# Optimization experiments

Measured on AMD Instinct MI355X. Metric: run time of the kernel, lower is better.

## Reference

```python
import jax, jax.numpy as jnp
import numpy as np

NUM_HEADS = 12
DIM = 768
NV = 4  # number of views
EPS = 1e-6


def _ln(x, g, b):
    m = x.mean(-1, keepdims=True)
    v = ((x - m) ** 2).mean(-1, keepdims=True)
    return (x - m) / jnp.sqrt(v + EPS) * g + b


def setup_inputs() -> dict:
    key = jax.random.key(0)
    ks = jax.random.split(key, 10)
    B, N, C, H = 4, 256, DIM, NUM_HEADS
    Hid = 4 * C
    s = 0.02
    return {
        'X': jax.random.normal(ks[0], (B * NV, N, C), jnp.float32),
        'norm1_g': jnp.ones((C,), jnp.float32),
        'norm1_b': jnp.zeros((C,), jnp.float32),
        'qkv_w': jax.random.normal(ks[1], (NV, 3 * C, C), jnp.float32) * s,
        'proj_w': jax.random.normal(ks[2], (NV, C, C), jnp.float32) * s,
        'proj_b': jnp.zeros((NV, C), jnp.float32),
        'norm2_g': jnp.ones((NV, C), jnp.float32),
        'norm2_b': jnp.zeros((NV, C), jnp.float32),
        'fc1_w': jax.random.normal(ks[3], (NV, Hid, C), jnp.float32) * s,
        'fc1_b': jnp.zeros((NV, Hid), jnp.float32),
        'fc2_w': jax.random.normal(ks[4], (NV, C, Hid), jnp.float32) * s,
        'fc2_b': jnp.zeros((NV, C), jnp.float32),
        'query': jax.random.normal(ks[5], (1, 1, C), jnp.float32),
        'mha_in_w': jax.random.normal(ks[6], (NV, 3 * C, C), jnp.float32) * s,
        'mha_in_b': jnp.zeros((NV, 3 * C), jnp.float32),
        'mha_out_w': jax.random.normal(ks[7], (NV, C, C), jnp.float32) * s,
        'mha_out_b': jnp.zeros((NV, C), jnp.float32),
    }


def reference(X, norm1_g, norm1_b, qkv_w, proj_w, proj_b, norm2_g, norm2_b,
              fc1_w, fc1_b, fc2_w, fc2_b, query, mha_in_w, mha_in_b,
              mha_out_w, mha_out_b):
    B4, N, C = X.shape
    B = B4 // NV
    H = NUM_HEADS
    hd = C // H
    scale = hd ** -0.5

    Xv = X.reshape(B, NV, N, C)
    Xn = _ln(Xv, norm1_g, norm1_b)

    # ---- FusionAttention: 4x4 pairwise cross attention between views ----
    qkv = jnp.einsum('bvnc,vdc->vbnd', Xn, qkv_w)              # [V,B,N,3C]
    qkv = qkv.reshape(NV, B, N, 3, H, hd).transpose(3, 0, 1, 4, 2, 5)  # [3,V,B,H,N,hd]
    q, k, v = qkv[0], qkv[1], qkv[2]
    scores = jnp.einsum('ibhnd,jbhmd->ijbhnm', q, k) * scale   # [V,V,B,H,N,N]
    attn = jax.nn.softmax(scores, axis=-1)
    ctx = jnp.einsum('ijbhnm,jbhmd->ijbhnd', attn, v)
    ctx = ctx.transpose(0, 1, 2, 4, 3, 5).reshape(NV, NV, B, N, C)
    # proj_i is affine, so mean over j of proj(x_j) == proj(mean_j x_j)
    ctx_mean = ctx.mean(axis=1)                                # [V,B,N,C]
    xa = jnp.einsum('vbnc,voc->vbno', ctx_mean, proj_w) + proj_b[:, None, None, :]

    x = xa * 2.0
    h = _ln(x, norm2_g[:, None, None, :], norm2_b[:, None, None, :])
    h1 = jax.nn.gelu(jnp.einsum('vbnc,vhc->vbnh', h, fc1_w) + fc1_b[:, None, None, :],
                     approximate=False)
    h2 = jnp.einsum('vbnh,vch->vbnc', h1, fc2_w) + fc2_b[:, None, None, :]
    x = x + h2                                                  # [V,B,N,C]

    # ---- CrossAttentionWithLearnableQuery (query identical for all T,B) ----
    wq, wk, wv = jnp.split(mha_in_w, 3, axis=1)                 # each [V,C,C]
    bq, bk, bv = jnp.split(mha_in_b, 3, axis=1)                 # each [V,C]
    q0 = query.reshape(C)
    qh = (jnp.einsum('c,vdc->vd', q0, wq) + bq).reshape(NV, H, hd)
    kh = (jnp.einsum('vbnc,vdc->vbnd', x, wk) + bk[:, None, None, :]).reshape(NV, B, N, H, hd)
    vh = (jnp.einsum('vbnc,vdc->vbnd', x, wv) + bv[:, None, None, :]).reshape(NV, B, N, H, hd)
    s2 = jnp.einsum('vhd,vbnhd->vbhn', qh, kh) * scale
    a2 = jax.nn.softmax(s2, axis=-1)
    c2 = jnp.einsum('vbhn,vbnhd->vbhd', a2, vh).reshape(NV, B, C)
    o = jnp.einsum('vbc,voc->vbo', c2, mha_out_w) + mha_out_b[:, None, :]  # [V,B,C]
    o = o.transpose(1, 0, 2).reshape(B, NV * C)                 # concat views
    # every query position produces identical output -> broadcast over T=N
    return jnp.broadcast_to(o[:, None, :], (B, N, NV * C))
```

## Files before the change

kernel.cpp:

```cpp
#include <hip/hip_runtime.h>
#include <math.h>

#define NVIEW 4
#define BATCH 4
#define NSEQ  256
#define CDIM  768
#define HEADS 12
#define HD    64

typedef __attribute__((ext_vector_type(8))) short   short8;
typedef __attribute__((ext_vector_type(8))) unsigned short ushort8;
typedef __attribute__((ext_vector_type(4))) float   float4v;

typedef const __attribute__((address_space(1))) void gas_t;
typedef       __attribute__((address_space(3))) void las_t;

__device__ __forceinline__ unsigned short f2b(float x)
{
    union { float f; unsigned u; } c; c.f = x;
    unsigned r = (c.u + 0x7FFFu + ((c.u >> 16) & 1u)) >> 16;
    return (unsigned short)r;
}

__device__ __forceinline__ unsigned pack2b(float a, float b)
{
    return (unsigned)f2b(a) | ((unsigned)f2b(b) << 16);
}

__device__ __forceinline__ void block_ln_row_b(const float* __restrict__ xrow,
                                               const float* __restrict__ g,
                                               const float* __restrict__ b,
                                               unsigned short* __restrict__ orow)
{
    const int t = threadIdx.x;
    float x0 = xrow[t], x1 = xrow[t + 256], x2 = xrow[t + 512];
    float s  = x0 + x1 + x2;
    float s2 = x0 * x0 + x1 * x1 + x2 * x2;
    #pragma unroll
    for (int off = 32; off > 0; off >>= 1) {
        s  += __shfl_down(s, off);
        s2 += __shfl_down(s2, off);
    }
    __shared__ float w1[4], w2[4];
    if ((t & 63) == 0) { w1[t >> 6] = s; w2[t >> 6] = s2; }
    __syncthreads();
    float S  = w1[0] + w1[1] + w1[2] + w1[3];
    float S2 = w2[0] + w2[1] + w2[2] + w2[3];
    float mean = S * (1.0f / 768.0f);
    float var  = S2 * (1.0f / 768.0f) - mean * mean;
    float inv  = rsqrtf(var + 1e-6f);
    orow[t]       = f2b((x0 - mean) * inv * g[t]       + b[t]);
    orow[t + 256] = f2b((x1 - mean) * inv * g[t + 256] + b[t + 256]);
    orow[t + 512] = f2b((x2 - mean) * inv * g[t + 512] + b[t + 512]);
}

__global__ void prologue(const float* __restrict__ X, const float* __restrict__ n1g,
                         const float* __restrict__ n1b, unsigned short* __restrict__ Xn,
                         const float* __restrict__ query, const float* __restrict__ Win,
                         const float* __restrict__ Bin, float* __restrict__ QH,
                         const float* __restrict__ qkv, const float* __restrict__ proj,
                         const float* __restrict__ fc1, const float* __restrict__ fc2,
                         const float* __restrict__ mha, unsigned short* __restrict__ wdst)
{
    const int bid = blockIdx.x;
    const int t   = threadIdx.x;

    if (bid < 4096) {
        const long NV8 = 4423680L;
        long vi = (long)bid * 256 + t;
        #pragma unroll 2
        for (; vi < NV8; vi += 4096L * 256) {
            long idx = vi * 8;
            const float* s;
            long base;
            if (idx < 7077888L)       { s = qkv;  base = 0; }
            else if (idx < 9437184L)  { s = proj; base = 7077888L; }
            else if (idx < 18874368L) { s = fc1;  base = 9437184L; }
            else if (idx < 28311552L) { s = fc2;  base = 18874368L; }
            else                      { s = mha;  base = 28311552L; }
            const float* sp = s + (idx - base);
            float4 a = *(const float4*)sp;
            float4 b = *(const float4*)(sp + 4);
            ushort8 o;
            o[0] = f2b(a.x); o[1] = f2b(a.y); o[2] = f2b(a.z); o[3] = f2b(a.w);
            o[4] = f2b(b.x); o[5] = f2b(b.y); o[6] = f2b(b.z); o[7] = f2b(b.w);
            *(ushort8*)(wdst + idx) = o;
        }
        return;
    }

    if (bid < 8192) {
        int rid = bid - 4096;
        int n  = rid & 255;
        int bv = rid >> 8;
        int bb = bv >> 2, v = bv & 3;
        const float* xrow = X + (long)rid * CDIM;
        unsigned short* orow = Xn + ((long)(v * 4 + bb) * 256 + n) * CDIM;
        block_ln_row_b(xrow, n1g, n1b, orow);
        return;
    }

    {
        const int bi   = bid - 8192;
        const int v    = bi / 192;
        const int dblk = bi - v * 192;
        const int wave = t >> 6;
        const int lane = t & 63;
        const int d    = dblk * 4 + wave;

        __shared__ float qs[768];
        for (int idx = t; idx < 768; idx += 256) qs[idx] = query[idx];
        __syncthreads();

        const float* w = Win + ((long)v * 2304 + d) * 768;
        float acc = 0.f;
        #pragma unroll
        for (int k = 0; k < 3; ++k) {
            int c = k * 256 + lane * 4;
            float4 w4 = *(const float4*)(w + c);
            float4 q4 = *(const float4*)&qs[c];
            acc += w4.x * q4.x + w4.y * q4.y + w4.z * q4.z + w4.w * q4.w;
        }
        #pragma unroll
        for (int off = 32; off > 0; off >>= 1) acc += __shfl_down(acc, off);
        if (lane == 0)
            QH[v * 768 + d] = acc + Bin[(long)v * 2304 + d];
    }
}

__global__ void ln2_kernel(const float* __restrict__ Xin, const float* __restrict__ g,
                           const float* __restrict__ b, unsigned short* __restrict__ Out)
{
    int rid = blockIdx.x;
    int v = rid >> 10;
    const float* xrow = Xin + (long)rid * CDIM;
    block_ln_row_b(xrow, g + v * CDIM, b + v * CDIM, Out + (long)rid * CDIM);
}

template <int EPI, int TM, int BK, typename OT>
__launch_bounds__(256, 3)
__global__ void gemm_bf16(const unsigned short* __restrict__ A,
                          const unsigned short* __restrict__ W,
                          const float* __restrict__ bias, const float* __restrict__ resid,
                          OT* __restrict__ out, int M, int N, int K,
                          long wStride, long wOff, int bStride, int bOff)
{
    const int nbx = gridDim.x, nby = gridDim.y;
    const int nwg = nbx * nby * (int)gridDim.z;
    const int orig = blockIdx.x + nbx * (blockIdx.y + nby * blockIdx.z);
    const int cpx = nwg >> 3;
    const int wid = (orig & 7) * cpx + (orig >> 3);
    const int bz  = wid / (nbx * nby);
    const int rr  = wid - bz * (nbx * nby);
    const int by  = rr / nbx;
    const int bx  = rr - by * nbx;

    const int v = bz;
    const unsigned short* Av = A + (long)v * M * K;
    const unsigned short* Wv = W + v * wStride + wOff;

    constexpr int CH  = BK / 8;
    constexpr int RPG = 512 / BK;

    __shared__ unsigned short As[TM * BK];
    __shared__ unsigned short Bs[128 * BK];

    const int tid  = threadIdx.x;
    const int lane = tid & 63;
    const int wave = tid >> 6;
    const int l15  = lane & 15;
    const int quad = lane >> 4;
    const int row0 = by * TM, col0 = bx * 128;

    constexpr int MI = 4;
    constexpr int NI = (TM == 128) ? 4 : 2;
    const int mw = (TM == 128) ? (wave & 1) * 64 : 0;
    const int nw = (TM == 128) ? (wave >> 1) * 64 : wave * 32;

    float4v acc[MI][NI];
    #pragma unroll
    for (int i = 0; i < MI; ++i)
        #pragma unroll
        for (int j = 0; j < NI; ++j)
            acc[i][j] = (float4v){0.f, 0.f, 0.f, 0.f};

    const int lr = lane / CH;
    const int pc = lane % CH;

    for (int k0 = 0; k0 < K; k0 += BK) {
        __syncthreads();
        #pragma unroll
        for (int g = 0; g < TM / (RPG * 4); ++g) {
            int G = wave * (TM / (RPG * 4)) + g;
            int r = G * RPG + lr;
            int c = pc ^ (r & 7);
            const unsigned short* sa = Av + (long)(row0 + r) * K + k0 + c * 8;
            __builtin_amdgcn_global_load_lds((gas_t*)sa, (las_t*)&As[G * 512], 16, 0, 0);
        }
        #pragma unroll
        for (int g = 0; g < 128 / (RPG * 4); ++g) {
            int G = wave * (128 / (RPG * 4)) + g;
            int r = G * RPG + lr;
            int c = pc ^ (r & 7);
            const unsigned short* sw = Wv + (long)(col0 + r) * K + k0 + c * 8;
            __builtin_amdgcn_global_load_lds((gas_t*)sw, (las_t*)&Bs[G * 512], 16, 0, 0);
        }
        __syncthreads();

        #pragma unroll
        for (int ks = 0; ks < BK / 32; ++ks) {
            short8 af[MI], bfr[NI];
            #pragma unroll
            for (int mi = 0; mi < MI; ++mi) {
                int m = mw + mi * 16 + l15;
                int p = (ks * 4 + quad) ^ (m & 7);
                af[mi] = *(const short8*)&As[m * BK + p * 8];
            }
            #pragma unroll
            for (int ni = 0; ni < NI; ++ni) {
                int n = nw + ni * 16 + l15;
                int p = (ks * 4 + quad) ^ (n & 7);
                bfr[ni] = *(const short8*)&Bs[n * BK + p * 8];
            }
            #pragma unroll
            for (int mi = 0; mi < MI; ++mi)
                #pragma unroll
                for (int ni = 0; ni < NI; ++ni)
                    acc[mi][ni] = __builtin_amdgcn_mfma_f32_16x16x32_bf16(af[mi], bfr[ni], acc[mi][ni], 0, 0, 0);
        }
    }

    #pragma unroll
    for (int mi = 0; mi < MI; ++mi) {
        #pragma unroll
        for (int ni = 0; ni < NI; ++ni) {
            int rowb = row0 + mw + mi * 16 + quad * 4;
            int col  = col0 + nw + ni * 16 + l15;
            float bval = 0.f;
            if (EPI >= 1) bval = bias[v * bStride + bOff + col];
            #pragma unroll
            for (int r = 0; r < 4; ++r) {
                float x = acc[mi][ni][r] + bval;
                long off = (long)v * M * N + (long)(rowb + r) * N + col;
                if constexpr (EPI == 2) {
                    x = 0.5f * x * (1.0f + erff(x * 0.70710678118654752f));
                } else if constexpr (EPI == 3) {
                    x += resid[off];
                } else if constexpr (EPI == 4) {
                    x *= 2.0f;
                }
                if constexpr (sizeof(OT) == 2) ((unsigned short*)out)[off] = f2b(x);
                else                           ((float*)out)[off] = x;
            }
        }
    }
}

__launch_bounds__(256, 3)
__global__ void fusion_attn_mfma(const unsigned short* __restrict__ QKV,
                                 unsigned short* __restrict__ ctx)
{
    const int qt = blockIdx.x;
    const int b  = blockIdx.y / HEADS;
    const int h  = blockIdx.y % HEADS;
    const int i  = blockIdx.z;
    const int tid  = threadIdx.x;
    const int lane = tid & 63;
    const int wave = tid >> 6;
    const int l15  = lane & 15;
    const int quad = lane >> 4;

    __shared__ unsigned short Qs[64 * 72];
    __shared__ unsigned short KVu[64 * 136];
    __shared__ unsigned short Ps[64 * 136];

    {
        int r = tid >> 2, p16 = (tid & 3) * 16;
        const unsigned short* src = QKV + ((long)((i * 4 + b) * 256 + qt * 64 + r)) * 2304 + h * 64 + p16;
        *(ushort8*)(&Qs[r * 72 + p16])     = *(const ushort8*)(src);
        *(ushort8*)(&Qs[r * 72 + p16 + 8]) = *(const ushort8*)(src + 8);
    }

    const int kg = tid & 31;
    const int dc = tid >> 5;

    float4v acc_o[4];
    #pragma unroll
    for (int e = 0; e < 4; ++e) acc_o[e] = (float4v){0.f, 0.f, 0.f, 0.f};

    for (int j = 0; j < 4; ++j) {
        const unsigned short* Kb = QKV + ((long)((j * 4 + b) * 256)) * 2304 + 768 + h * 64;
        const unsigned short* Vb = Kb + 768;

        float4v sacc[16];
        #pragma unroll
        for (int t = 0; t < 16; ++t) sacc[t] = (float4v){0.f, 0.f, 0.f, 0.f};

        ushort8 vv0[4], vv1[4];

        __syncthreads();
        #pragma unroll
        for (int g = 0; g < 4; ++g) {
            int R = wave * 32 + g * 8;
            int r = R + (lane >> 3);
            int p = lane & 7;
            int c = (p - (r & 7)) & 7;
            const unsigned short* src = Kb + (long)(r) * 2304 + c * 8;
            __builtin_amdgcn_global_load_lds((gas_t*)src, (las_t*)&KVu[R * 64], 16, 0, 0);
        }
        __syncthreads();
        __builtin_amdgcn_s_setprio(1);
        #pragma unroll
        for (int ks = 0; ks < 2; ++ks) {
            int lcq = ks * 4 + quad;
            short8 qf = *(const short8*)&Qs[(wave * 16 + l15) * 72 + lcq * 8];
            #pragma unroll
            for (int nn = 0; nn < 8; ++nn) {
                int n = nn * 16 + l15;
                int p = (lcq + (n & 7)) & 7;
                short8 kf = *(const short8*)&KVu[n * 64 + p * 8];
                sacc[nn] = __builtin_amdgcn_mfma_f32_16x16x32_bf16(kf, qf, sacc[nn], 0, 0, 0);
            }
        }
        __builtin_amdgcn_s_setprio(0);

        __syncthreads();
        #pragma unroll
        for (int g = 0; g < 4; ++g) {
            int R = wave * 32 + g * 8;
            int r = R + (lane >> 3);
            int p = lane & 7;
            int c = (p - (r & 7)) & 7;
            const unsigned short* src = Kb + (long)(128 + r) * 2304 + c * 8;
            __builtin_amdgcn_global_load_lds((gas_t*)src, (las_t*)&KVu[R * 64], 16, 0, 0);
        }
        __builtin_amdgcn_sched_barrier(0);
        #pragma unroll
        for (int q = 0; q < 4; ++q)
            vv0[q] = *(const ushort8*)(Vb + (long)(kg * 4 + q) * 2304 + dc * 8);
        asm volatile("s_waitcnt vmcnt(4) lgkmcnt(0)" ::: "memory");
        __builtin_amdgcn_s_barrier();
        __builtin_amdgcn_sched_barrier(0);
        __builtin_amdgcn_s_setprio(1);
        #pragma unroll
        for (int ks = 0; ks < 2; ++ks) {
            int lcq = ks * 4 + quad;
            short8 qf = *(const short8*)&Qs[(wave * 16 + l15) * 72 + lcq * 8];
            #pragma unroll
            for (int nn = 0; nn < 8; ++nn) {
                int n = nn * 16 + l15;
                int p = (lcq + (n & 7)) & 7;
                short8 kf = *(const short8*)&KVu[n * 64 + p * 8];
                sacc[8 + nn] = __builtin_amdgcn_mfma_f32_16x16x32_bf16(kf, qf, sacc[8 + nn], 0, 0, 0);
            }
        }
        __builtin_amdgcn_s_setprio(0);

        float m = -1e30f;
        #pragma unroll
        for (int t = 0; t < 16; ++t)
            #pragma unroll
            for (int r = 0; r < 4; ++r) {
                sacc[t][r] *= 0.125f;
                m = fmaxf(m, sacc[t][r]);
            }
        m = fmaxf(m, __shfl_xor(m, 16));
        m = fmaxf(m, __shfl_xor(m, 32));
        float lsum = 0.f;
        #pragma unroll
        for (int t = 0; t < 16; ++t)
            #pragma unroll
            for (int r = 0; r < 4; ++r) {
                float e = __expf(sacc[t][r] - m);
                sacc[t][r] = e;
                lsum += e;
            }
        lsum += __shfl_xor(lsum, 16);
        lsum += __shfl_xor(lsum, 32);
        float invl = 1.0f / lsum;

        float4v pv[4];
        #pragma unroll
        for (int e = 0; e < 4; ++e) pv[e] = (float4v){0.f, 0.f, 0.f, 0.f};

        __syncthreads();
        #pragma unroll
        for (int nn = 0; nn < 8; ++nn) {
            unsigned lo = pack2b(sacc[nn][0], sacc[nn][1]);
            unsigned hi = pack2b(sacc[nn][2], sacc[nn][3]);
            *(unsigned long long*)&Ps[(wave * 16 + l15) * 136 + nn * 16 + quad * 4] =
                ((unsigned long long)hi << 32) | lo;
        }
        #pragma unroll
        for (int jj = 0; jj < 8; ++jj) {
            unsigned lo = (unsigned)vv0[0][jj] | ((unsigned)vv0[1][jj] << 16);
            unsigned hi = (unsigned)vv0[2][jj] | ((unsigned)vv0[3][jj] << 16);
            *(unsigned long long*)&KVu[(dc * 8 + jj) * 136 + kg * 4] =
                ((unsigned long long)hi << 32) | lo;
        }
        #pragma unroll
        for (int q = 0; q < 4; ++q)
            vv1[q] = *(const ushort8*)(Vb + (long)(128 + kg * 4 + q) * 2304 + dc * 8);
        asm volatile("s_waitcnt lgkmcnt(0)" ::: "memory");
        __builtin_amdgcn_s_barrier();
        __builtin_amdgcn_sched_barrier(0);
        __builtin_amdgcn_s_setprio(1);
        #pragma unroll
        for (int ks = 0; ks < 4; ++ks) {
            int lc = ks * 4 + quad;
            short8 pf = *(const short8*)&Ps[(wave * 16 + l15) * 136 + lc * 8];
            #pragma unroll
            for (int et = 0; et < 4; ++et) {
                short8 vf = *(const short8*)&KVu[(et * 16 + l15) * 136 + lc * 8];
                pv[et] = __builtin_amdgcn_mfma_f32_16x16x32_bf16(vf, pf, pv[et], 0, 0, 0);
            }
        }
        __builtin_amdgcn_s_setprio(0);

        __syncthreads();
        #pragma unroll
        for (int nn = 0; nn < 8; ++nn) {
            unsigned lo = pack2b(sacc[8 + nn][0], sacc[8 + nn][1]);
            unsigned hi = pack2b(sacc[8 + nn][2], sacc[8 + nn][3]);
            *(unsigned long long*)&Ps[(wave * 16 + l15) * 136 + nn * 16 + quad * 4] =
                ((unsigned long long)hi << 32) | lo;
        }
        #pragma unroll
        for (int jj = 0; jj < 8; ++jj) {
            unsigned lo = (unsigned)vv1[0][jj] | ((unsigned)vv1[1][jj] << 16);
            unsigned hi = (unsigned)vv1[2][jj] | ((unsigned)vv1[3][jj] << 16);
            *(unsigned long long*)&KVu[(dc * 8 + jj) * 136 + kg * 4] =
                ((unsigned long long)hi << 32) | lo;
        }
        __syncthreads();
        __builtin_amdgcn_s_setprio(1);
        #pragma unroll
        for (int ks = 0; ks < 4; ++ks) {
            int lc = ks * 4 + quad;
            short8 pf = *(const short8*)&Ps[(wave * 16 + l15) * 136 + lc * 8];
            #pragma unroll
            for (int et = 0; et < 4; ++et) {
                short8 vf = *(const short8*)&KVu[(et * 16 + l15) * 136 + lc * 8];
                pv[et] = __builtin_amdgcn_mfma_f32_16x16x32_bf16(vf, pf, pv[et], 0, 0, 0);
            }
        }
        __builtin_amdgcn_s_setprio(0);

        #pragma unroll
        for (int et = 0; et < 4; ++et)
            #pragma unroll
            for (int r = 0; r < 4; ++r)
                acc_o[et][r] += pv[et][r] * invl;
    }

    #pragma unroll
    for (int et = 0; et < 4; ++et) {
        unsigned lo = pack2b(acc_o[et][0] * 0.25f, acc_o[et][1] * 0.25f);
        unsigned hi = pack2b(acc_o[et][2] * 0.25f, acc_o[et][3] * 0.25f);
        long row = (long)((i * 4 + b) * 256 + qt * 64 + wave * 16 + l15);
        int  col = h * 64 + et * 16 + quad * 4;
        *(unsigned long long*)&ctx[row * 768 + col] = ((unsigned long long)hi << 32) | lo;
    }
}

__launch_bounds__(256, 2)
__global__ void cross_attn(const float* __restrict__ KVH, const float* __restrict__ QH,
                           float* __restrict__ C2)
{
    const int h = blockIdx.x, b = blockIdx.y, v = blockIdx.z;
    const int t = threadIdx.x;
    __shared__ float qv[64];
    __shared__ float p[256];
    __shared__ float part[4][64];
    __shared__ float wred[4], wred2[4];

    if (t < 64) qv[t] = QH[(v * 12 + h) * 64 + t];
    __syncthreads();

    const float* krow = KVH + ((long)((v * 4 + b) * 256 + t)) * 1536 + h * 64;
    float s = 0.f;
    #pragma unroll
    for (int e = 0; e < 64; e += 4) {
        float4 k4 = *(const float4*)(krow + e);
        s += qv[e] * k4.x + qv[e + 1] * k4.y + qv[e + 2] * k4.z + qv[e + 3] * k4.w;
    }
    s *= 0.125f;
    float m4 = s;
    #pragma unroll
    for (int off = 32; off > 0; off >>= 1) m4 = fmaxf(m4, __shfl_down(m4, off));
    if ((t & 63) == 0) wred[t >> 6] = m4;
    __syncthreads();
    float rmax = fmaxf(fmaxf(wred[0], wred[1]), fmaxf(wred[2], wred[3]));
    float ev = __expf(s - rmax);
    p[t] = ev;
    float s4 = ev;
    #pragma unroll
    for (int off = 32; off > 0; off >>= 1) s4 += __shfl_down(s4, off);
    if ((t & 63) == 0) wred2[t >> 6] = s4;
    __syncthreads();
    float inv = 1.0f / (wred2[0] + wred2[1] + wred2[2] + wred2[3]);

    const int e = t & 63, ch = t >> 6;
    const float* vbase = KVH + ((long)((v * 4 + b) * 256)) * 1536 + 768 + h * 64 + e;
    float accv = 0.f;
    for (int m = ch * 64; m < ch * 64 + 64; ++m)
        accv += p[m] * vbase[(long)m * 1536];
    part[ch][e] = accv;
    __syncthreads();
    if (t < 64)
        C2[(v * 4 + b) * 768 + h * 64 + t] =
            (part[0][t] + part[1][t] + part[2][t] + part[3][t]) * inv;
}

__launch_bounds__(256, 4)
__global__ void out_matvec(const float* __restrict__ C2, const float* __restrict__ Wout,
                           const float* __restrict__ Bout, float* __restrict__ obc)
{
    const int bi   = blockIdx.x;
    const int v    = bi / 192;
    const int dblk = bi - v * 192;
    const int t    = threadIdx.x;
    const int wave = t >> 6;
    const int lane = t & 63;
    const int d    = dblk * 4 + wave;

    __shared__ float c2s[3072];
    #pragma unroll
    for (int idx = 0; idx < 3072; idx += 256) c2s[idx + t] = C2[v * 3072 + idx + t];
    __syncthreads();

    const float* w = Wout + ((long)v * 768 + d) * 768;
    float acc0 = 0.f, acc1 = 0.f, acc2 = 0.f, acc3 = 0.f;
    #pragma unroll
    for (int k = 0; k < 3; ++k) {
        int c = k * 256 + lane * 4;
        float4 w4 = *(const float4*)(w + c);
        float4 a0 = *(const float4*)&c2s[c];
        float4 a1 = *(const float4*)&c2s[768 + c];
        float4 a2 = *(const float4*)&c2s[1536 + c];
        float4 a3 = *(const float4*)&c2s[2304 + c];
        acc0 += w4.x * a0.x + w4.y * a0.y + w4.z * a0.z + w4.w * a0.w;
        acc1 += w4.x * a1.x + w4.y * a1.y + w4.z * a1.z + w4.w * a1.w;
        acc2 += w4.x * a2.x + w4.y * a2.y + w4.z * a2.z + w4.w * a2.w;
        acc3 += w4.x * a3.x + w4.y * a3.y + w4.z * a3.z + w4.w * a3.w;
    }
    #pragma unroll
    for (int off = 32; off > 0; off >>= 1) {
        acc0 += __shfl_down(acc0, off);
        acc1 += __shfl_down(acc1, off);
        acc2 += __shfl_down(acc2, off);
        acc3 += __shfl_down(acc3, off);
    }
    if (lane == 0) {
        float bb = Bout[v * 768 + d];
        obc[0 * 3072 + v * 768 + d] = acc0 + bb;
        obc[1 * 3072 + v * 768 + d] = acc1 + bb;
        obc[2 * 3072 + v * 768 + d] = acc2 + bb;
        obc[3 * 3072 + v * 768 + d] = acc3 + bb;
    }
}

__launch_bounds__(256, 4)
__global__ void out_bcast(const float* __restrict__ obc, float* __restrict__ out)
{
    const int b  = blockIdx.x >> 6;
    const int n0 = (blockIdx.x & 63) * 4;
    const int t  = threadIdx.x;
    const float4* src = (const float4*)(obc + (long)b * 3072);
    float4 v0 = src[t], v1 = src[t + 256], v2 = src[t + 512];
    float4* dst = (float4*)(out + ((long)(b * 256 + n0)) * 3072);
    #pragma unroll
    for (int r = 0; r < 4; ++r) {
        dst[r * 768 + t]       = v0;
        dst[r * 768 + t + 256] = v1;
        dst[r * 768 + t + 512] = v2;
    }
}

extern "C" void kernel_launch(void* const* d_in, const int* in_sizes, int n_in,
                              void* d_out, int out_size, void* d_ws, size_t ws_size,
                              hipStream_t stream)
{
    const float* X        = (const float*)d_in[0];
    const float* n1g      = (const float*)d_in[1];
    const float* n1b      = (const float*)d_in[2];
    const float* qkv_w    = (const float*)d_in[3];
    const float* proj_w   = (const float*)d_in[4];
    const float* proj_b   = (const float*)d_in[5];
    const float* n2g      = (const float*)d_in[6];
    const float* n2b      = (const float*)d_in[7];
    const float* fc1_w    = (const float*)d_in[8];
    const float* fc1_b    = (const float*)d_in[9];
    const float* fc2_w    = (const float*)d_in[10];
    const float* fc2_b    = (const float*)d_in[11];
    const float* query    = (const float*)d_in[12];
    const float* mha_in_w = (const float*)d_in[13];
    const float* mha_in_b = (const float*)d_in[14];
    const float* mha_out_w= (const float*)d_in[15];
    const float* mha_out_b= (const float*)d_in[16];
    float* out = (float*)d_out;

    char* wsb = (char*)d_ws;
    unsigned short* wbuf = (unsigned short*)wsb;
    unsigned short* rgA  = (unsigned short*)(wsb + 70778880);
    char*           rgB  = wsb + 77070336;
    float*          xbuf = (float*)(wsb + 102236160);
    float*          qh   = (float*)(wsb + 114819072);
    float*          c2   = (float*)(wsb + 114831360);
    float*          obc  = (float*)(wsb + 114880512);

    unsigned short* QKV = (unsigned short*)rgB;
    unsigned short* H1  = (unsigned short*)rgB;
    float*          KVH = (float*)rgB;

    prologue<<<8960, 256, 0, stream>>>(X, n1g, n1b, rgA,
                                       query, mha_in_w, mha_in_b, qh,
                                       qkv_w, proj_w, fc1_w, fc2_w, mha_in_w, wbuf);
    gemm_bf16<0, 128, 64, unsigned short><<<dim3(18, 8, 4), 256, 0, stream>>>(
        rgA, wbuf, nullptr, nullptr, QKV, 1024, 2304, 768, 2304L * 768, 0, 0, 0);
    fusion_attn_mfma<<<dim3(4, 48, 4), 256, 0, stream>>>(QKV, rgA);
    gemm_bf16<4, 64, 128, float><<<dim3(6, 16, 4), 256, 0, stream>>>(
        rgA, wbuf + 7077888, proj_b, nullptr, xbuf, 1024, 768, 768, 768L * 768, 0, 768, 0);
    ln2_kernel<<<4096, 256, 0, stream>>>(xbuf, n2g, n2b, rgA);
    gemm_bf16<2, 128, 64, unsigned short><<<dim3(24, 8, 4), 256, 0, stream>>>(
        rgA, wbuf + 9437184, fc1_b, nullptr, H1, 1024, 3072, 768, 3072L * 768, 0, 3072, 0);
    gemm_bf16<3, 64, 128, unsigned short><<<dim3(6, 16, 4), 256, 0, stream>>>(
        H1, wbuf + 18874368, fc2_b, xbuf, rgA, 1024, 768, 3072, 768L * 3072, 0, 768, 0);
    gemm_bf16<1, 64, 128, float><<<dim3(12, 16, 4), 256, 0, stream>>>(
        rgA, wbuf + 28311552, mha_in_b, nullptr, KVH, 1024, 1536, 768, 2304L * 768, 768L * 768, 2304, 768);
    cross_attn<<<dim3(12, 4, 4), 256, 0, stream>>>(KVH, qh, c2);
    out_matvec<<<768, 256, 0, stream>>>(c2, mha_out_w, mha_out_b, obc);
    out_bcast<<<256, 256, 0, stream>>>(obc, out);
}
```

Baseline: 393.6 us.

## Overlap bulk weight conversion with the QKV GEMM in one launch

Split the weight fp32-to-bf16 conversion so only qkv weights are converted in the prologue. The proj, fc1, fc2 and mha weights are converted by extra blocks appended to a new specialised QKV GEMM kernel, so that memory-bound work runs concurrently with the compute-bound GEMM. The GEMM is a hardcoded single-buffered version of the templated one. This risks the extra blocks competing for bandwidth and CU slots with the GEMM.

```diff
diff --git a/kernel.cpp b/kernel.cpp
--- a/kernel.cpp
+++ b/kernel.cpp
@@ -58,23 +58,99 @@
                          const float* __restrict__ n1b, unsigned short* __restrict__ Xn,
                          const float* __restrict__ query, const float* __restrict__ Win,
                          const float* __restrict__ Bin, float* __restrict__ QH,
-                         const float* __restrict__ qkv, const float* __restrict__ proj,
-                         const float* __restrict__ fc1, const float* __restrict__ fc2,
-                         const float* __restrict__ mha, unsigned short* __restrict__ wdst)
+                         const float* __restrict__ qkv, unsigned short* __restrict__ wdst)
 {
     const int bid = blockIdx.x;
     const int t   = threadIdx.x;
 
-    if (bid < 4096) {
-        const long NV8 = 4423680L;
+    if (bid < 1024) {
+        const long NV8 = 884736L;
         long vi = (long)bid * 256 + t;
         #pragma unroll 2
-        for (; vi < NV8; vi += 4096L * 256) {
+        for (; vi < NV8; vi += 1024L * 256) {
+            long idx = vi * 8;
+            const float* sp = qkv + idx;
+            float4 a = *(const float4*)sp;
+            float4 b = *(const float4*)(sp + 4);
+            ushort8 o;
+            o[0] = f2b(a.x); o[1] = f2b(a.y); o[2] = f2b(a.z); o[3] = f2b(a.w);
+            o[4] = f2b(b.x); o[5] = f2b(b.y); o[6] = f2b(b.z); o[7] = f2b(b.w);
+            *(ushort8*)(wdst + idx) = o;
+        }
+        return;
+    }
+
+    if (bid < 5120) {
+        int rid = bid - 1024;
+        int n  = rid & 255;
+        int bv = rid >> 8;
+        int bb = bv >> 2, v = bv & 3;
+        const float* xrow = X + (long)rid * CDIM;
+        unsigned short* orow = Xn + ((long)(v * 4 + bb) * 256 + n) * CDIM;
+        block_ln_row_b(xrow, n1g, n1b, orow);
+        return;
+    }
+
+    {
+        const int bi   = bid - 5120;
+        const int v    = bi / 192;
+        const int dblk = bi - v * 192;
+        const int wave = t >> 6;
+        const int lane = t & 63;
+        const int d    = dblk * 4 + wave;
+
+        __shared__ float qs[768];
+        for (int idx = t; idx < 768; idx += 256) qs[idx] = query[idx];
+        __syncthreads();
+
+        const float* w = Win + ((long)v * 2304 + d) * 768;
+        float acc = 0.f;
+        #pragma unroll
+        for (int k = 0; k < 3; ++k) {
+            int c = k * 256 + lane * 4;
+            float4 w4 = *(const float4*)(w + c);
+            float4 q4 = *(const float4*)&qs[c];
+            acc += w4.x * q4.x + w4.y * q4.y + w4.z * q4.z + w4.w * q4.w;
+        }
+        #pragma unroll
+        for (int off = 32; off > 0; off >>= 1) acc += __shfl_down(acc, off);
+        if (lane == 0)
+            QH[v * 768 + d] = acc + Bin[(long)v * 2304 + d];
+    }
+}
+
+__global__ void ln2_kernel(const float* __restrict__ Xin, const float* __restrict__ g,
+                           const float* __restrict__ b, unsigned short* __restrict__ Out)
+{
+    int rid = blockIdx.x;
+    int v = rid >> 10;
+    const float* xrow = Xin + (long)rid * CDIM;
+    block_ln_row_b(xrow, g + v * CDIM, b + v * CDIM, Out + (long)rid * CDIM);
+}
+
+__launch_bounds__(256, 3)
+__global__ void qkv_conv(const unsigned short* __restrict__ A,
+                         const unsigned short* __restrict__ W,
+                         unsigned short* __restrict__ out,
+                         const float* __restrict__ proj, const float* __restrict__ fc1,
+                         const float* __restrict__ fc2, const float* __restrict__ mha,
+                         unsigned short* __restrict__ wdst)
+{
+    __shared__ unsigned short As[128 * 64];
+    __shared__ unsigned short Bs[128 * 64];
+
+    const int bid = blockIdx.x;
+    const int tid = threadIdx.x;
+
+    if (bid >= 576) {
+        const long C0  = 884736L;
+        const long CN  = 4423680L;
+        long vi = C0 + (long)(bid - 576) * 256 + tid;
+        for (; vi < CN; vi += 1024L * 256) {
             long idx = vi * 8;
             const float* s;
             long base;
-            if (idx < 7077888L)       { s = qkv;  base = 0; }
-            else if (idx < 9437184L)  { s = proj; base = 7077888L; }
+            if (idx < 9437184L)       { s = proj; base = 7077888L; }
             else if (idx < 18874368L) { s = fc1;  base = 9437184L; }
             else if (idx < 28311552L) { s = fc2;  base = 18874368L; }
             else                      { s = mha;  base = 28311552L; }
@@ -89,52 +165,95 @@
         return;
     }
 
-    if (bid < 8192) {
-        int rid = bid - 4096;
-        int n  = rid & 255;
-        int bv = rid >> 8;
-        int bb = bv >> 2, v = bv & 3;
-        const float* xrow = X + (long)rid * CDIM;
-        unsigned short* orow = Xn + ((long)(v * 4 + bb) * 256 + n) * CDIM;
-        block_ln_row_b(xrow, n1g, n1b, orow);
-        return;
-    }
-
-    {
-        const int bi   = bid - 8192;
-        const int v    = bi / 192;
-        const int dblk = bi - v * 192;
-        const int wave = t >> 6;
-        const int lane = t & 63;
-        const int d    = dblk * 4 + wave;
-
-        __shared__ float qs[768];
-        for (int idx = t; idx < 768; idx += 256) qs[idx] = query[idx];
-        __syncthreads();
-
-        const float* w = Win + ((long)v * 2304 + d) * 768;
-        float acc = 0.f;
-        #pragma unroll
-        for (int k = 0; k < 3; ++k) {
-            int c = k * 256 + lane * 4;
-            float4 w4 = *(const float4*)(w + c);
-            float4 q4 = *(const float4*)&qs[c];
-            acc += w4.x * q4.x + w4.y * q4.y + w4.z * q4.z + w4.w * q4.w;
-        }
-        #pragma unroll
-        for (int off = 32; off > 0; off >>= 1) acc += __shfl_down(acc, off);
-        if (lane == 0)
-            QH[v * 768 + d] = acc + Bin[(long)v * 2304 + d];
-    }
-}
-
-__global__ void ln2_kernel(const float* __restrict__ Xin, const float* __restrict__ g,
-                           const float* __restrict__ b, unsigned short* __restrict__ Out)
-{
-    int rid = blockIdx.x;
-    int v = rid >> 10;
-    const float* xrow = Xin + (long)rid * CDIM;
-    block_ln_row_b(xrow, g + v * CDIM, b + v * CDIM, Out + (long)rid * CDIM);
+    constexpr int M = 1024, N = 2304, K = 768;
+    constexpr int nbx = 18, nby = 8, nwg = 576, cpx = nwg >> 3;
+
+    const int orig = bid;
+    const int wid = (orig & 7) * cpx + (orig >> 3);
+    const int bz  = wid / (nbx * nby);
+    const int rr  = wid - bz * (nbx * nby);
+    const int by  = rr / nbx;
+    const int bx  = rr - by * nbx;
+
+    const int v = bz;
+    const unsigned short* Av = A + (long)v * M * K;
+    const unsigned short* Wv = W + (long)v * N * K;
+
+    const int lane = tid & 63;
+    const int wave = tid >> 6;
+    const int l15  = lane & 15;
+    const int quad = lane >> 4;
+    const int row0 = by * 128, col0 = bx * 128;
+
+    const int mw = (wave & 1) * 64;
+    const int nw = (wave >> 1) * 64;
+
+    float4v acc[4][4];
+    #pragma unroll
+    for (int i = 0; i < 4; ++i)
+        #pragma unroll
+        for (int j = 0; j < 4; ++j)
+            acc[i][j] = (float4v){0.f, 0.f, 0.f, 0.f};
+
+    const int lr = lane >> 3;
+    const int pc = lane & 7;
+
+    for (int k0 = 0; k0 < K; k0 += 64) {
+        __syncthreads();
+        #pragma unroll
+        for (int g = 0; g < 4; ++g) {
+            int G = wave * 4 + g;
+            int r = G * 8 + lr;
+            int c = pc ^ (r & 7);
+            const unsigned short* sa = Av + (long)(row0 + r) * K + k0 + c * 8;
+            __builtin_amdgcn_global_load_lds((gas_t*)sa, (las_t*)&As[G * 512], 16, 0, 0);
+        }
+        #pragma unroll
+        for (int g = 0; g < 4; ++g) {
+            int G = wave * 4 + g;
+            int r = G * 8 + lr;
+            int c = pc ^ (r & 7);
+            const unsigned short* sw = Wv + (long)(col0 + r) * K + k0 + c * 8;
+            __builtin_amdgcn_global_load_lds((gas_t*)sw, (las_t*)&Bs[G * 512], 16, 0, 0);
+        }
+        __syncthreads();
+
+        #pragma unroll
+        for (int ks = 0; ks < 2; ++ks) {
+            short8 af[4], bfr[4];
+            #pragma unroll
+            for (int mi = 0; mi < 4; ++mi) {
+                int m = mw + mi * 16 + l15;
+                int p = (ks * 4 + quad) ^ (m & 7);
+                af[mi] = *(const short8*)&As[m * 64 + p * 8];
+            }
+            #pragma unroll
+            for (int ni = 0; ni < 4; ++ni) {
+                int n = nw + ni * 16 + l15;
+                int p = (ks * 4 + quad) ^ (n & 7);
+                bfr[ni] = *(const short8*)&Bs[n * 64 + p * 8];
+            }
+            #pragma unroll
+            for (int mi = 0; mi < 4; ++mi)
+                #pragma unroll
+                for (int ni = 0; ni < 4; ++ni)
+                    acc[mi][ni] = __builtin_amdgcn_mfma_f32_16x16x32_bf16(af[mi], bfr[ni], acc[mi][ni], 0, 0, 0);
+        }
+    }
+
+    #pragma unroll
+    for (int mi = 0; mi < 4; ++mi) {
+        #pragma unroll
+        for (int ni = 0; ni < 4; ++ni) {
+            int rowb = row0 + mw + mi * 16 + quad * 4;
+            int col  = col0 + nw + ni * 16 + l15;
+            #pragma unroll
+            for (int r = 0; r < 4; ++r) {
+                long off = (long)v * M * N + (long)(rowb + r) * N + col;
+                out[off] = f2b(acc[mi][ni][r]);
+            }
+        }
+    }
 }
 
 template <int EPI, int TM, int BK, typename OT>
@@ -613,11 +732,11 @@
     unsigned short* H1  = (unsigned short*)rgB;
     float*          KVH = (float*)rgB;
 
-    prologue<<<8960, 256, 0, stream>>>(X, n1g, n1b, rgA,
+    prologue<<<5888, 256, 0, stream>>>(X, n1g, n1b, rgA,
                                        query, mha_in_w, mha_in_b, qh,
-                                       qkv_w, proj_w, fc1_w, fc2_w, mha_in_w, wbuf);
-    gemm_bf16<0, 128, 64, unsigned short><<<dim3(18, 8, 4), 256, 0, stream>>>(
-        rgA, wbuf, nullptr, nullptr, QKV, 1024, 2304, 768, 2304L * 768, 0, 0, 0);
+                                       qkv_w, wbuf);
+    qkv_conv<<<1600, 256, 0, stream>>>(rgA, wbuf, QKV,
+                                       proj_w, fc1_w, fc2_w, mha_in_w, wbuf);
     fusion_attn_mfma<<<dim3(4, 48, 4), 256, 0, stream>>>(QKV, rgA);
     gemm_bf16<4, 64, 128, float><<<dim3(6, 16, 4), 256, 0, stream>>>(
         rgA, wbuf + 7077888, proj_b, nullptr, xbuf, 1024, 768, 768, 768L * 768, 0, 768, 0);
```

After: 400.0 us. No clear change (+1.6%).
